# Optimization experiments

Measured on AMD Instinct MI355X. Metric: run time of the kernel, lower is better.

Reference implementation:

```python
import jax, jax.numpy as jnp
import numpy as np

EPS = 1e-12  # F.normalize default eps


def _l2_normalize(x, axis):
    n = jnp.sqrt(jnp.sum(x * x, axis=axis, keepdims=True))
    return x / jnp.maximum(n, EPS)


def setup_inputs() -> dict:
    key = jax.random.key(0)
    k1, k2 = jax.random.split(key)
    code = jax.random.normal(k1, (8, 768, 32, 32), dtype=jnp.float32)
    clusters = jax.random.normal(k2, (64, 768), dtype=jnp.float32)
    return {"code": code, "clusters": clusters, "image_hw": 512}


def reference(code, clusters, image_hw):
    # L2-normalize cluster centroids over channel dim and features over C
    normed_clusters = _l2_normalize(clusters, axis=1)            # [N, C]
    normed_features = _l2_normalize(code, axis=1)                # [B, C, H, W]
    # cosine similarity to every cluster
    inner_products = jnp.einsum('bchw,nc->bnhw', normed_features, normed_clusters)  # [B,N,H,W]
    # hard nearest-cluster assignment -> one-hot over N (channel axis 1)
    assign = jnp.argmax(inner_products, axis=1)                  # [B, H, W] int
    n_classes = clusters.shape[0]
    cluster_probs = jnp.moveaxis(
        jax.nn.one_hot(assign, n_classes, dtype=jnp.float32), -1, 1)  # [B,N,H,W]
    # training loss: negative mean of selected (max) similarity
    cluster_loss = -jnp.mean(jnp.sum(cluster_probs * inner_products, axis=1))
    # resize_to(cluster_probs, image): bilinear upsample to image resolution
    B, N = cluster_probs.shape[0], cluster_probs.shape[1]
    resized = jax.image.resize(cluster_probs, (B, N, image_hw, image_hw), method='bilinear')
    return (cluster_loss, resized, code)
```

## Files before the change

### kernel.cpp

```cpp
#include <hip/hip_runtime.h>

#define CCH 768
#define NCL 64
#define HWIN 1024
#define RES_ELEMS 134217728LL
#define CODE_ELEMS 6291456LL
#define CQUADS 1572863LL
#define ASSIGN_BLOCKS 256
#define COPY_BLOCKS2 512
#define DENSE_BLOCKS 2048

__global__ __launch_bounds__(256) void k_assign(const float* __restrict__ code,
                                                const float* __restrict__ clusters,
                                                int* __restrict__ assign,
                                                float* __restrict__ loss_part,
                                                float* __restrict__ out)
{
    int tid = threadIdx.x;
    int blk = blockIdx.x;

    if (blk >= ASSIGN_BLOCKS) {
        long long u = (long long)(blk - ASSIGN_BLOCKS) * 256 + tid;
        #pragma unroll
        for (int k = 0; k < 12; ++k) {
            long long q = u + (long long)k * (COPY_BLOCKS2 * 256);
            if (q < CQUADS) {
                const float* src = code + 3 + 4 * q;
                float4 v = make_float4(src[0], src[1], src[2], src[3]);
                *(float4*)(out + RES_ELEMS + 4 + 4 * q) = v;
            }
        }
        if (blk == ASSIGN_BLOCKS && tid == 0) {
            out[RES_ELEMS + 1] = code[0];
            out[RES_ELEMS + 2] = code[1];
            out[RES_ELEMS + 3] = code[2];
            out[RES_ELEMS + CODE_ELEMS] = code[CODE_ELEMS - 1];
        }
        return;
    }

    __shared__ float lds_nc[64 * 64];
    __shared__ float lds_red[4 * 2048];
    __shared__ float lds_sq[4 * 32];
    __shared__ float s_scale[64];

    int lane = tid & 63;
    int w = tid >> 6;

    for (int t = 0; t < 16; ++t) {
        int n = w * 16 + t;
        const float* row = clusters + n * CCH;
        float ss = 0.f;
        #pragma unroll
        for (int j = 0; j < 3; ++j) {
            float4 v = *(const float4*)(row + 4 * (lane + 64 * j));
            ss += v.x * v.x + v.y * v.y + v.z * v.z + v.w * v.w;
        }
        #pragma unroll
        for (int m = 1; m < 64; m <<= 1) ss += __shfl_xor(ss, m);
        if (lane == 0) s_scale[n] = 1.0f / fmaxf(sqrtf(ss), 1e-12f);
    }
    __syncthreads();

    int cg = tid >> 5;
    int ng = (tid >> 3) & 3;
    int pg = tid & 7;
    int b = blk >> 5;
    int pixb = (blk & 31) << 5;
    const float* codeB = code + (size_t)b * CCH * HWIN + pixb + (pg << 2);

    int n2 = tid >> 2;
    int qq = tid & 3;
    float myscale = s_scale[n2];

    float acc[4][16];
    #pragma unroll
    for (int p = 0; p < 4; ++p)
        #pragma unroll
        for (int q = 0; q < 16; ++q) acc[p][q] = 0.f;
    float sq0 = 0.f, sq1 = 0.f, sq2 = 0.f, sq3 = 0.f;

    for (int k = 0; k < 12; ++k) {
        __syncthreads();
        const float* srcrow = clusters + n2 * CCH + k * 64 + qq * 16;
        #pragma unroll
        for (int i = 0; i < 4; ++i) {
            float4 v = *(const float4*)(srcrow + 4 * i);
            lds_nc[(qq * 16 + 4 * i + 0) * 64 + n2] = v.x * myscale;
            lds_nc[(qq * 16 + 4 * i + 1) * 64 + n2] = v.y * myscale;
            lds_nc[(qq * 16 + 4 * i + 2) * 64 + n2] = v.z * myscale;
            lds_nc[(qq * 16 + 4 * i + 3) * 64 + n2] = v.w * myscale;
        }
        __syncthreads();
        #pragma unroll
        for (int m = 0; m < 8; ++m) {
            int ch = k * 64 + cg * 8 + m;
            float4 f = *(const float4*)(codeB + (size_t)ch * HWIN);
            sq0 += f.x * f.x; sq1 += f.y * f.y; sq2 += f.z * f.z; sq3 += f.w * f.w;
            const float* ncrow = lds_nc + ((cg * 8 + m) << 6) + (ng << 4);
            #pragma unroll
            for (int q = 0; q < 16; ++q) {
                float w2 = ncrow[q];
                acc[0][q] += f.x * w2;
                acc[1][q] += f.y * w2;
                acc[2][q] += f.z * w2;
                acc[3][q] += f.w * w2;
            }
        }
    }

    #pragma unroll
    for (int p = 0; p < 4; ++p)
        #pragma unroll
        for (int q = 0; q < 16; ++q)
            acc[p][q] += __shfl_xor(acc[p][q], 32);
    sq0 += __shfl_xor(sq0, 32);
    sq1 += __shfl_xor(sq1, 32);
    sq2 += __shfl_xor(sq2, 32);
    sq3 += __shfl_xor(sq3, 32);

    if ((tid & 32) == 0) {
        #pragma unroll
        for (int p = 0; p < 4; ++p) {
            float4* dstp = (float4*)&lds_red[w * 2048 + (pg * 4 + p) * 64 + ng * 16];
            dstp[0] = make_float4(acc[p][0],  acc[p][1],  acc[p][2],  acc[p][3]);
            dstp[1] = make_float4(acc[p][4],  acc[p][5],  acc[p][6],  acc[p][7]);
            dstp[2] = make_float4(acc[p][8],  acc[p][9],  acc[p][10], acc[p][11]);
            dstp[3] = make_float4(acc[p][12], acc[p][13], acc[p][14], acc[p][15]);
        }
        if (ng == 0) {
            lds_sq[w * 32 + pg * 4 + 0] = sq0;
            lds_sq[w * 32 + pg * 4 + 1] = sq1;
            lds_sq[w * 32 + pg * 4 + 2] = sq2;
            lds_sq[w * 32 + pg * 4 + 3] = sq3;
        }
    }
    __syncthreads();

    for (int idx = tid; idx < 2048; idx += 256) {
        float s = 0.f;
        #pragma unroll
        for (int c2 = 0; c2 < 4; ++c2) s += lds_red[c2 * 2048 + idx];
        lds_nc[idx] = s;
    }
    __syncthreads();

    if (tid < 32) {
        float ss = 0.f;
        #pragma unroll
        for (int c2 = 0; c2 < 4; ++c2) ss += lds_sq[c2 * 32 + tid];
        float inv = 1.0f / fmaxf(sqrtf(ss), 1e-12f);
        float best = -1e30f; int bi = 0;
        for (int n = 0; n < 64; ++n) {
            float v = lds_nc[tid * 64 + n];
            if (v > best) { best = v; bi = n; }
        }
        assign[blk * 32 + tid] = bi;
        float l = best * inv;
        l += __shfl_down(l, 16);
        l += __shfl_down(l, 8);
        l += __shfl_down(l, 4);
        l += __shfl_down(l, 2);
        l += __shfl_down(l, 1);
        if (tid == 0) loss_part[blk] = -l * (1.0f / 8192.0f);
    }
}

__global__ __launch_bounds__(256) void k_dense(const int* __restrict__ assign,
                                               const float* __restrict__ loss_part,
                                               float* __restrict__ out)
{
    int tid = threadIdx.x;
    int blk = blockIdx.x;

    if (blk == 0) {
        __shared__ float lr[4];
        float v = loss_part[tid];
        #pragma unroll
        for (int m = 1; m < 64; m <<= 1) v += __shfl_xor(v, m);
        if ((tid & 63) == 0) lr[tid >> 6] = v;
        __syncthreads();
        if (tid == 0) out[0] = lr[0] + lr[1] + lr[2] + lr[3];
    }

    int b =  blk >> 8;
    int n = (blk >> 2) & 63;
    int c =  blk & 3;
    int I0 = c << 7;
    int rbase = (I0 >> 4) - 1;

    __shared__ unsigned s_mask[10];
    __shared__ int4   s_jj[128];
    __shared__ float4 s_fj[128];

    int lane = tid & 63;
    int w = tid >> 6;

    {
        int r = (w << 1) + (lane >> 5);
        int ir = rbase + r; ir = ir < 0 ? 0 : (ir > 31 ? 31 : ir);
        bool pred = assign[(b << 10) + (ir << 5) + (lane & 31)] == n;
        unsigned long long m = __ballot(pred);
        if (lane == 0) { s_mask[(w << 1)] = (unsigned)m; s_mask[(w << 1) + 1] = (unsigned)(m >> 32); }
    }
    if (w == 0) {
        int r = 8 + (lane >> 5);
        int ir = rbase + r; ir = ir < 0 ? 0 : (ir > 31 ? 31 : ir);
        bool pred = assign[(b << 10) + (ir << 5) + (lane & 31)] == n;
        unsigned long long m = __ballot(pred);
        if (lane == 0) { s_mask[8] = (unsigned)m; s_mask[9] = (unsigned)(m >> 32); }
    }

    if (tid < 128) {
        int s = tid;
        int jl[4];
        if (s == 0) { jl[0] = 0; jl[1] = 1; jl[2] = 2; jl[3] = 511; }
        else { jl[0] = 4 * s - 1; jl[1] = 4 * s; jl[2] = 4 * s + 1; jl[3] = 4 * s + 2; }
        int pj[4]; float fjv[4];
        #pragma unroll
        for (int k = 0; k < 4; ++k) {
            int j = jl[k];
            float xj = (j + 0.5f) * 0.0625f - 0.5f;
            float fjf = floorf(xj);
            int jj = (int)fjf;
            fjv[k] = xj - fjf;
            int j0 = jj < 0 ? 0 : jj;
            int j1 = (jj + 1) > 31 ? 31 : (jj + 1);
            pj[k] = j0 | (j1 << 8);
        }
        s_jj[s] = make_int4(pj[0], pj[1], pj[2], pj[3]);
        s_fj[s] = make_float4(fjv[0], fjv[1], fjv[2], fjv[3]);
    }
    __syncthreads();

    int rr = tid >> 7;
    int s  = tid & 127;
    int4   pj4 = s_jj[s];
    float4 fj4 = s_fj[s];
    int   j0a[4] = { pj4.x & 255, pj4.y & 255, pj4.z & 255, pj4.w & 255 };
    int   j1a[4] = { pj4.x >> 8,  pj4.y >> 8,  pj4.z >> 8,  pj4.w >> 8 };
    float fja[4] = { fj4.x, fj4.y, fj4.z, fj4.w };

    long long planebase = 1LL + ((long long)b << 24) + ((long long)n << 18);

    for (int r2 = 0; r2 < 64; ++r2) {
        int i = I0 + (r2 << 1) + rr;
        float xi = (i + 0.5f) * 0.0625f - 0.5f;
        float fif = floorf(xi);
        int ii = (int)fif;
        float fi = xi - fif;
        float fi1 = 1.0f - fi;
        unsigned m0 = s_mask[ii - rbase];
        unsigned m1 = s_mask[ii - rbase + 1];
        float v[4];
        #pragma unroll
        for (int k = 0; k < 4; ++k) {
            float b00 = (float)((m0 >> j0a[k]) & 1u);
            float b01 = (float)((m0 >> j1a[k]) & 1u);
            float b10 = (float)((m1 >> j0a[k]) & 1u);
            float b11 = (float)((m1 >> j1a[k]) & 1u);
            float P = fi1 * b00 + fi * b10;
            float Q = fi1 * b01 + fi * b11;
            v[k] = P + fja[k] * (Q - P);
        }
        float* rowbase = out + planebase + ((long long)i << 9);
        if (s == 0) {
            rowbase[0] = v[0]; rowbase[1] = v[1]; rowbase[2] = v[2]; rowbase[511] = v[3];
        } else {
            *(float4*)(rowbase + 4 * s - 1) = make_float4(v[0], v[1], v[2], v[3]);
        }
    }
}

extern "C" void kernel_launch(void* const* d_in, const int* in_sizes, int n_in,
                              void* d_out, int out_size, void* d_ws, size_t ws_size,
                              hipStream_t stream)
{
    const float* code     = (const float*)d_in[0];
    const float* clusters = (const float*)d_in[1];
    float* out = (float*)d_out;
    int* assign = (int*)d_ws;
    float* loss_part = (float*)((char*)d_ws + 32768);

    k_assign<<<ASSIGN_BLOCKS + COPY_BLOCKS2, 256, 0, stream>>>(code, clusters, assign, loss_part, out);
    k_dense <<<DENSE_BLOCKS,                 256, 0, stream>>>(assign, loss_part, out);
}
```

Baseline: 612.2 us.

## Split assignment kernel into 1024 blocks of 8 pixels each

The nearest-cluster assignment kernel now gives each block 8 pixels instead of 32, which quadruples the grid to 1024 blocks. Each thread accumulates a 4x4 tile instead of 4x16, and the cross-wave reduction and loss reduction are adjusted to match, so that more CUs are busy and register pressure drops. In exchange, each block reloads and renormalizes the full cluster matrix into LDS, so cluster traffic and normalization work grow fourfold, and the code loads are narrower per pixel row.

```diff
diff --git a/kernel.cpp b/kernel.cpp
--- a/kernel.cpp
+++ b/kernel.cpp
@@ -6,7 +6,7 @@
 #define RES_ELEMS 134217728LL
 #define CODE_ELEMS 6291456LL
 #define CQUADS 1572863LL
-#define ASSIGN_BLOCKS 256
+#define ASSIGN_BLOCKS 1024
 #define COPY_BLOCKS2 512
 #define DENSE_BLOCKS 2048
 
@@ -40,8 +40,8 @@
     }
 
     __shared__ float lds_nc[64 * 64];
-    __shared__ float lds_red[4 * 2048];
-    __shared__ float lds_sq[4 * 32];
+    __shared__ float lds_red[4 * 512];
+    __shared__ float lds_sq[4 * 8];
     __shared__ float s_scale[64];
 
     int lane = tid & 63;
@@ -63,21 +63,21 @@
     __syncthreads();
 
     int cg = tid >> 5;
-    int ng = (tid >> 3) & 3;
-    int pg = tid & 7;
-    int b = blk >> 5;
-    int pixb = (blk & 31) << 5;
-    const float* codeB = code + (size_t)b * CCH * HWIN + pixb + (pg << 2);
+    int ng = (tid >> 1) & 15;
+    int pg = tid & 1;
+    int b  = blk >> 7;
+    int po = (blk & 127) << 3;
+    const float* codeB = code + (size_t)b * CCH * HWIN + po + (pg << 2);
 
     int n2 = tid >> 2;
     int qq = tid & 3;
     float myscale = s_scale[n2];
 
-    float acc[4][16];
+    float acc[4][4];
     #pragma unroll
     for (int p = 0; p < 4; ++p)
         #pragma unroll
-        for (int q = 0; q < 16; ++q) acc[p][q] = 0.f;
+        for (int q = 0; q < 4; ++q) acc[p][q] = 0.f;
     float sq0 = 0.f, sq1 = 0.f, sq2 = 0.f, sq3 = 0.f;
 
     for (int k = 0; k < 12; ++k) {
@@ -97,10 +97,11 @@
             int ch = k * 64 + cg * 8 + m;
             float4 f = *(const float4*)(codeB + (size_t)ch * HWIN);
             sq0 += f.x * f.x; sq1 += f.y * f.y; sq2 += f.z * f.z; sq3 += f.w * f.w;
-            const float* ncrow = lds_nc + ((cg * 8 + m) << 6) + (ng << 4);
+            float4 wv = *(const float4*)(lds_nc + ((cg * 8 + m) << 6) + (ng << 2));
+            float wl[4] = { wv.x, wv.y, wv.z, wv.w };
             #pragma unroll
-            for (int q = 0; q < 16; ++q) {
-                float w2 = ncrow[q];
+            for (int q = 0; q < 4; ++q) {
+                float w2 = wl[q];
                 acc[0][q] += f.x * w2;
                 acc[1][q] += f.y * w2;
                 acc[2][q] += f.z * w2;
@@ -112,7 +113,7 @@
     #pragma unroll
     for (int p = 0; p < 4; ++p)
         #pragma unroll
-        for (int q = 0; q < 16; ++q)
+        for (int q = 0; q < 4; ++q)
             acc[p][q] += __shfl_xor(acc[p][q], 32);
     sq0 += __shfl_xor(sq0, 32);
     sq1 += __shfl_xor(sq1, 32);
@@ -120,45 +121,41 @@
     sq3 += __shfl_xor(sq3, 32);
 
     if ((tid & 32) == 0) {
-        #pragma unroll
-        for (int p = 0; p < 4; ++p) {
-            float4* dstp = (float4*)&lds_red[w * 2048 + (pg * 4 + p) * 64 + ng * 16];
-            dstp[0] = make_float4(acc[p][0],  acc[p][1],  acc[p][2],  acc[p][3]);
-            dstp[1] = make_float4(acc[p][4],  acc[p][5],  acc[p][6],  acc[p][7]);
-            dstp[2] = make_float4(acc[p][8],  acc[p][9],  acc[p][10], acc[p][11]);
-            dstp[3] = make_float4(acc[p][12], acc[p][13], acc[p][14], acc[p][15]);
-        }
+        int sub = tid & 31;
+        float* d = &lds_red[w * 512 + sub * 16];
+        *(float4*)(d + 0)  = make_float4(acc[0][0], acc[0][1], acc[0][2], acc[0][3]);
+        *(float4*)(d + 4)  = make_float4(acc[1][0], acc[1][1], acc[1][2], acc[1][3]);
+        *(float4*)(d + 8)  = make_float4(acc[2][0], acc[2][1], acc[2][2], acc[2][3]);
+        *(float4*)(d + 12) = make_float4(acc[3][0], acc[3][1], acc[3][2], acc[3][3]);
         if (ng == 0) {
-            lds_sq[w * 32 + pg * 4 + 0] = sq0;
-            lds_sq[w * 32 + pg * 4 + 1] = sq1;
-            lds_sq[w * 32 + pg * 4 + 2] = sq2;
-            lds_sq[w * 32 + pg * 4 + 3] = sq3;
-        }
-    }
-    __syncthreads();
-
-    for (int idx = tid; idx < 2048; idx += 256) {
-        float s = 0.f;
-        #pragma unroll
-        for (int c2 = 0; c2 < 4; ++c2) s += lds_red[c2 * 2048 + idx];
-        lds_nc[idx] = s;
-    }
-    __syncthreads();
-
-    if (tid < 32) {
-        float ss = 0.f;
-        #pragma unroll
-        for (int c2 = 0; c2 < 4; ++c2) ss += lds_sq[c2 * 32 + tid];
+            lds_sq[w * 8 + pg * 4 + 0] = sq0;
+            lds_sq[w * 8 + pg * 4 + 1] = sq1;
+            lds_sq[w * 8 + pg * 4 + 2] = sq2;
+            lds_sq[w * 8 + pg * 4 + 3] = sq3;
+        }
+    }
+    __syncthreads();
+
+    for (int idx = tid; idx < 512; idx += 256) {
+        int px = idx >> 6, n = idx & 63;
+        int ng2 = n >> 2, q = n & 3;
+        int pg2 = px >> 2, p = px & 3;
+        int off = (ng2 * 2 + pg2) * 16 + p * 4 + q;
+        float s = lds_red[off] + lds_red[512 + off] + lds_red[1024 + off] + lds_red[1536 + off];
+        lds_nc[px * 64 + n] = s;
+    }
+    __syncthreads();
+
+    if (tid < 8) {
+        float ss = lds_sq[tid] + lds_sq[8 + tid] + lds_sq[16 + tid] + lds_sq[24 + tid];
         float inv = 1.0f / fmaxf(sqrtf(ss), 1e-12f);
         float best = -1e30f; int bi = 0;
         for (int n = 0; n < 64; ++n) {
             float v = lds_nc[tid * 64 + n];
             if (v > best) { best = v; bi = n; }
         }
-        assign[blk * 32 + tid] = bi;
+        assign[blk * 8 + tid] = bi;
         float l = best * inv;
-        l += __shfl_down(l, 16);
-        l += __shfl_down(l, 8);
         l += __shfl_down(l, 4);
         l += __shfl_down(l, 2);
         l += __shfl_down(l, 1);
@@ -175,7 +172,8 @@
 
     if (blk == 0) {
         __shared__ float lr[4];
-        float v = loss_part[tid];
+        float v = loss_part[tid] + loss_part[tid + 256]
+                + loss_part[tid + 512] + loss_part[tid + 768];
         #pragma unroll
         for (int m = 1; m < 64; m <<= 1) v += __shfl_xor(v, m);
         if ((tid & 63) == 0) lr[tid >> 6] = v;
```

Measured after the change: 618.9 us. Within noise of the previous version (+1.1%).
